# Performance work log

Hardware: AMD Instinct MI355X
Metric: run time of the kernel (lower is better)

The kernel has to match this reference:

```python
import jax, jax.numpy as jnp
import numpy as np

HIDDEN = 4096
N_HEADS = 32
N_KV = 8
HEAD_DIM = 128
ROPE_BASE = 10000.0


def setup_inputs() -> dict:
    key = jax.random.key(0)
    k0, k1, k2, k3, k4 = jax.random.split(key, 5)
    B, S = 1, 2048
    scale = 0.02
    return {
        "hidden_states": jax.random.normal(k0, (B, S, HIDDEN), dtype=jnp.float32),
        "Wq": jax.random.normal(k1, (N_HEADS * HEAD_DIM, HIDDEN), dtype=jnp.float32) * scale,
        "Wk": jax.random.normal(k2, (N_KV * HEAD_DIM, HIDDEN), dtype=jnp.float32) * scale,
        "Wv": jax.random.normal(k3, (N_KV * HEAD_DIM, HIDDEN), dtype=jnp.float32) * scale,
        "Wo": jax.random.normal(k4, (HIDDEN, N_HEADS * HEAD_DIM), dtype=jnp.float32) * scale,
    }


def _rotate_half(x):
    x1, x2 = jnp.split(x, 2, axis=-1)
    return jnp.concatenate([-x2, x1], axis=-1)


def _rope_cos_sin(seq_len, dtype):
    inv_freq = 1.0 / (ROPE_BASE ** (jnp.arange(0, HEAD_DIM, 2, dtype=jnp.float32) / HEAD_DIM))
    t = jnp.arange(seq_len, dtype=jnp.float32)
    freqs = jnp.outer(t, inv_freq)                 # [S, hd/2]
    emb = jnp.concatenate([freqs, freqs], axis=-1) # [S, hd]
    return jnp.cos(emb).astype(dtype), jnp.sin(emb).astype(dtype)


def reference(hidden_states, Wq, Wk, Wv, Wo):
    B, S, _ = hidden_states.shape
    scale = HEAD_DIM ** -0.5
    groups = N_HEADS // N_KV

    q = (hidden_states @ Wq.T).reshape(B, S, N_HEADS, HEAD_DIM).transpose(0, 2, 1, 3)
    k = (hidden_states @ Wk.T).reshape(B, S, N_KV, HEAD_DIM).transpose(0, 2, 1, 3)
    v = (hidden_states @ Wv.T).reshape(B, S, N_KV, HEAD_DIM).transpose(0, 2, 1, 3)

    cos, sin = _rope_cos_sin(S, q.dtype)           # [S, hd] each, broadcast over (B, H)
    q = q * cos + _rotate_half(q) * sin
    k = k * cos + _rotate_half(k) * sin

    # repeat_kv: [B, nkv, S, hd] -> [B, nkv*groups, S, hd]
    k = jnp.broadcast_to(k[:, :, None], (B, N_KV, groups, S, HEAD_DIM)).reshape(B, N_HEADS, S, HEAD_DIM)
    v = jnp.broadcast_to(v[:, :, None], (B, N_KV, groups, S, HEAD_DIM)).reshape(B, N_HEADS, S, HEAD_DIM)

    scores = jnp.einsum('bhqd,bhkd->bhqk', q, k) * scale
    causal = jnp.tril(jnp.ones((S, S), dtype=bool))
    scores = jnp.where(causal, scores, -jnp.inf)
    probs = jax.nn.softmax(scores.astype(jnp.float32), axis=-1).astype(q.dtype)

    attn = jnp.einsum('bhqk,bhkd->bhqd', probs, v)            # [B, H, S, hd]
    attn = attn.transpose(0, 2, 1, 3).reshape(B, S, N_HEADS * HEAD_DIM)
    return attn @ Wo.T
```

## Files before the change

kernel.cpp:

```cpp
#include <hip/hip_runtime.h>
#include <hip/hip_bf16.h>
#include <math.h>

#define S_LEN 2048
#define HIDDEN 4096
#define N_HEADS 32
#define N_KV 8
#define HEAD_DIM 128

typedef __attribute__((ext_vector_type(8))) short short8;
typedef __attribute__((ext_vector_type(4))) float f32x4;

typedef __attribute__((address_space(3))) unsigned int as3_u32;
typedef const __attribute__((address_space(1))) unsigned int as1_u32;

__device__ __forceinline__ void gload16(const void* g, void* lds) {
  __builtin_amdgcn_global_load_lds((as1_u32*)g, (as3_u32*)lds, 16, 0, 0);
}

__device__ __forceinline__ unsigned short f2bf(float f) {
  unsigned int u = __float_as_uint(f);
  return (unsigned short)((u + 0x7fff + ((u >> 16) & 1)) >> 16);
}
__device__ __forceinline__ float bf2f(unsigned short u) {
  return __uint_as_float(((unsigned int)u) << 16);
}

__global__ void conv_bf16(const float* __restrict__ in, unsigned short* __restrict__ out, int n) {
  int i = (blockIdx.x * blockDim.x + threadIdx.x) * 4;
  if (i >= n) return;
  float4 v = *(const float4*)&in[i];
  ushort4 o;
  o.x = f2bf(v.x); o.y = f2bf(v.y); o.z = f2bf(v.z); o.w = f2bf(v.w);
  *(ushort4*)&out[i] = o;
}

__device__ __forceinline__ void storeC(float* C, float v) { *C = v; }
__device__ __forceinline__ void storeC(unsigned short* C, float v) { *C = f2bf(v); }

template <typename OutT>
__device__ __forceinline__ void gemm_core_128(
    const unsigned short* __restrict__ A, const unsigned short* __restrict__ B,
    OutT* __restrict__ C, int K, int ldc) {
  __shared__ unsigned short As[128 * 32];
  __shared__ unsigned short Bs[128 * 32];

  const int tid = threadIdx.x;
  const int w = tid >> 6;
  const int lane = tid & 63;
  const int wr = (w >> 1) * 64;
  const int wc = (w & 1) * 64;
  const int lrow = lane & 15;
  const int lk8 = lane >> 4;

  f32x4 acc[4][4];
#pragma unroll
  for (int i = 0; i < 4; i++)
#pragma unroll
    for (int j = 0; j < 4; j++) acc[i][j] = (f32x4){0.f, 0.f, 0.f, 0.f};

  const int sr = (lane >> 2);
  const int sc = (lane & 3) * 8;

  for (int k0 = 0; k0 < K; k0 += 32) {
    __syncthreads();
#pragma unroll
    for (int s = 0; s < 2; s++) {
      int r = w * 32 + s * 16 + sr;
      gload16(&A[(size_t)r * K + k0 + sc], &As[(w * 32 + s * 16) * 32]);
      gload16(&B[(size_t)r * K + k0 + sc], &Bs[(w * 32 + s * 16) * 32]);
    }
    __syncthreads();

    short8 a[4], b[4];
#pragma unroll
    for (int i = 0; i < 4; i++)
      a[i] = *(const short8*)&As[(wr + i * 16 + lrow) * 32 + lk8 * 8];
#pragma unroll
    for (int j = 0; j < 4; j++)
      b[j] = *(const short8*)&Bs[(wc + j * 16 + lrow) * 32 + lk8 * 8];
#pragma unroll
    for (int i = 0; i < 4; i++)
#pragma unroll
      for (int j = 0; j < 4; j++)
        acc[i][j] = __builtin_amdgcn_mfma_f32_16x16x32_bf16(a[i], b[j], acc[i][j], 0, 0, 0);
  }

#pragma unroll
  for (int i = 0; i < 4; i++)
#pragma unroll
    for (int j = 0; j < 4; j++) {
      int col = wc + j * 16 + lrow;
#pragma unroll
      for (int r = 0; r < 4; r++) {
        int row = wr + i * 16 + lk8 * 4 + r;
        storeC(&C[(size_t)row * ldc + col], acc[i][j][r]);
      }
    }
}

__global__ __launch_bounds__(256) void gemm_qkv(
    const unsigned short* __restrict__ Xb,
    const unsigned short* __restrict__ Wqb, const unsigned short* __restrict__ Wkb,
    const unsigned short* __restrict__ Wvb,
    unsigned short* __restrict__ Qb, unsigned short* __restrict__ Kb,
    unsigned short* __restrict__ Vb) {
  const int colBase = blockIdx.x * 128;
  const int rowBase = blockIdx.y * 128;
  const unsigned short* B;
  unsigned short* C;
  int ldc, ccol;
  if (colBase < 4096)      { B = Wqb + (size_t)colBase * HIDDEN;          C = Qb; ldc = 4096; ccol = colBase; }
  else if (colBase < 5120) { B = Wkb + (size_t)(colBase - 4096) * HIDDEN; C = Kb; ldc = 1024; ccol = colBase - 4096; }
  else                     { B = Wvb + (size_t)(colBase - 5120) * HIDDEN; C = Vb; ldc = 1024; ccol = colBase - 5120; }
  gemm_core_128(Xb + (size_t)rowBase * HIDDEN, B,
                C + (size_t)rowBase * ldc + ccol, HIDDEN, ldc);
}

__global__ __launch_bounds__(256) void gemm_out(
    const unsigned short* __restrict__ Ob, const unsigned short* __restrict__ Wob,
    float* __restrict__ C) {
  const int colBase = blockIdx.x * 128;
  const int rowBase = blockIdx.y * 128;
  gemm_core_128(Ob + (size_t)rowBase * HIDDEN, Wob + (size_t)colBase * HIDDEN,
                C + (size_t)rowBase * HIDDEN + colBase, HIDDEN, HIDDEN);
}

#define QSCALE 0.12753102123752056f

__global__ void rope_kernel(const unsigned short* __restrict__ Q,
                            const unsigned short* __restrict__ K,
                            unsigned short* __restrict__ Qp,
                            unsigned short* __restrict__ Kp) {
  int idx = blockIdx.x * blockDim.x + threadIdx.x;
  int d = idx & 63;
  int sh = idx >> 6;
  int h = sh % (N_HEADS + N_KV);
  int s = sh / (N_HEADS + N_KV);
  if (s >= S_LEN) return;

  float freq = expf(-(float)d * (9.210340371976184f / 64.0f));
  float ang = (float)s * freq;
  float sn, cs;
  sincosf(ang, &sn, &cs);

  const unsigned short* src;
  unsigned short* dst;
  float sc_out;
  if (h < N_HEADS) {
    src = Q + ((size_t)s * N_HEADS + h) * HEAD_DIM;
    dst = Qp + (((size_t)h * 128 + (s >> 4)) * 16 + (s & 15)) * HEAD_DIM;
    sc_out = QSCALE;
  } else {
    int kvh = h - N_HEADS;
    src = K + ((size_t)s * N_KV + kvh) * HEAD_DIM;
    dst = Kp + (((size_t)kvh * 32 + (s >> 6)) * 64 + (s & 63)) * HEAD_DIM;
    sc_out = 1.0f;
  }

  float x1 = bf2f(src[d]);
  float x2 = bf2f(src[d + 64]);
  dst[d] = f2bf((x1 * cs - x2 * sn) * sc_out);
  dst[d + 64] = f2bf((x2 * cs + x1 * sn) * sc_out);
}

__global__ __launch_bounds__(256) void transp_v(
    const unsigned short* __restrict__ Vb, unsigned short* __restrict__ Vp) {
  __shared__ unsigned short t[64][72];
  const int s0 = blockIdx.x * 64;
  const int c0 = blockIdx.y * 64;
  const int kt = s0 >> 6;
  const int tid = threadIdx.x;
#pragma unroll
  for (int i = 0; i < 2; i++) {
    int c = tid + i * 256;
    int r = c >> 3, ch = c & 7;
    *(short8*)&t[r][ch * 8] = *(const short8*)&Vb[(size_t)(s0 + r) * 1024 + c0 + ch * 8];
  }
  __syncthreads();
#pragma unroll
  for (int i = 0; i < 4; i++) {
    int c = tid + i * 256;
    int orow = c >> 4, oc4 = (c & 15) * 4;
    int g = c0 + orow;
    int kvh = g >> 7, d = g & 127;
    ushort4 o;
    o.x = t[oc4 + 0][orow]; o.y = t[oc4 + 1][orow];
    o.z = t[oc4 + 2][orow]; o.w = t[oc4 + 3][orow];
    *(ushort4*)&Vp[(((size_t)kvh * 32 + kt) * 128 + d) * 64 + oc4] = o;
  }
}

#define AK 64

__global__ __launch_bounds__(256, 4) void attn_mfma(
    const unsigned short* __restrict__ Qp, const unsigned short* __restrict__ Kp,
    const unsigned short* __restrict__ Vp, unsigned short* __restrict__ Ob) {
  const int b = blockIdx.x;
  const int h = b & 31;
  const int j = b >> 5;
  const int qt = (b < 512) ? j : (47 - j);
  const int kvh = h >> 2;

  const int tid = threadIdx.x;
  const int w = tid >> 6;
  const int lane = tid & 63;
  const int lrow = lane & 15;
  const int lk8 = lane >> 4;

  __shared__ unsigned short Ks[64 * 128];
  __shared__ unsigned short Vts[128 * 64];
  __shared__ unsigned short Ps[4 * 16 * 64];
  unsigned short* Pw = &Ps[w * 16 * 64];

  short8 qf[4];
  const int t0 = qt * 4 + w;
#pragma unroll
  for (int ks = 0; ks < 4; ks++)
    qf[ks] = *(const short8*)&Qp[(((size_t)h * 128 + t0) * 16 + lrow) * 128 +
                                 ks * 32 + lk8 * 8];

  f32x4 acc[8];
  float m_i = -1e30f, l_i = 0.f;
#pragma unroll
  for (int n = 0; n < 8; n++) acc[n] = (f32x4){0.f, 0.f, 0.f, 0.f};

  const int nkt = qt + 1;

  for (int kt = 0; kt < nkt; kt++) {
    const int kb = kt * AK;
    const unsigned short* Kt  = Kp + ((size_t)kvh * 32 + kt) * 8192;
    const unsigned short* Vtt = Vp + ((size_t)kvh * 32 + kt) * 8192;

    __syncthreads();
#pragma unroll
    for (int jj = 0; jj < 4; jj++) {
      int seg = w * 4 + jj;
      int kr = seg * 4 + lk8;
      int kc = lrow ^ (kr & 15);
      gload16(Kt + ((size_t)kr * 16 + kc) * 8, &Ks[seg * 512]);
      int vr = seg * 8 + (lane >> 3);
      int vc = (lane & 7) ^ (vr & 7);
      gload16(Vtt + ((size_t)vr * 8 + vc) * 8, &Vts[seg * 512]);
    }
    __syncthreads();

    f32x4 s[4];
#pragma unroll
    for (int n = 0; n < 4; n++) s[n] = (f32x4){0.f, 0.f, 0.f, 0.f};

#pragma unroll
    for (int ks = 0; ks < 4; ks++) {
      short8 kf[4];
#pragma unroll
      for (int n = 0; n < 4; n++)
        kf[n] = *(const short8*)&Ks[(n * 16 + lrow) * 128 + (((ks * 4 + lk8) ^ lrow)) * 8];
#pragma unroll
      for (int n = 0; n < 4; n++)
        s[n] = __builtin_amdgcn_mfma_f32_16x16x32_bf16(kf[n], qf[ks], s[n], 0, 0, 0);
    }

    const int wqb = qt * 64 + w * 16;
    if (kb + AK - 1 > wqb) {
      int query = wqb + lrow;
#pragma unroll
      for (int n = 0; n < 4; n++) {
        int keyb = kb + n * 16 + lk8 * 4;
#pragma unroll
        for (int r = 0; r < 4; r++)
          if (keyb + r > query) s[n][r] = -1e30f;
      }
    }

    {
      float mx = -1e30f;
#pragma unroll
      for (int n = 0; n < 4; n++)
#pragma unroll
        for (int r = 0; r < 4; r++) mx = fmaxf(mx, s[n][r]);
      mx = fmaxf(mx, __shfl_xor(mx, 16, 64));
      mx = fmaxf(mx, __shfl_xor(mx, 32, 64));
      float mn = fmaxf(m_i, mx);
      float al = exp2f(m_i - mn);
      m_i = mn;
      float ls = 0.f;
#pragma unroll
      for (int n = 0; n < 4; n++)
#pragma unroll
        for (int r = 0; r < 4; r++) {
          float e = exp2f(s[n][r] - mn);
          s[n][r] = e;
          ls += e;
        }
      ls += __shfl_xor(ls, 16, 64);
      ls += __shfl_xor(ls, 32, 64);
      l_i = l_i * al + ls;
#pragma unroll
      for (int n = 0; n < 8; n++)
#pragma unroll
        for (int r = 0; r < 4; r++) acc[n][r] *= al;
    }

#pragma unroll
    for (int n = 0; n < 4; n++) {
      ushort4 pk;
      pk.x = f2bf(s[n][0]); pk.y = f2bf(s[n][1]);
      pk.z = f2bf(s[n][2]); pk.w = f2bf(s[n][3]);
      int c8 = n * 4 + lk8;
      int c16s = (c8 >> 1) ^ (lrow & 7);
      *(ushort4*)&Pw[lrow * 64 + c16s * 8 + (c8 & 1) * 4] = pk;
    }

#pragma unroll
    for (int ks2 = 0; ks2 < 2; ks2++) {
      int c16s = (ks2 * 4 + lk8) ^ (lrow & 7);
      short8 pf = *(const short8*)&Pw[lrow * 64 + c16s * 8];
#pragma unroll
      for (int n = 0; n < 8; n++) {
        short8 vf = *(const short8*)&Vts[(n * 16 + lrow) * 64 +
                                         (((ks2 * 4 + lk8) ^ (lrow & 7))) * 8];
        acc[n] = __builtin_amdgcn_mfma_f32_16x16x32_bf16(vf, pf, acc[n], 0, 0, 0);
      }
    }
  }

  {
    float inv = 1.0f / l_i;
    int row = qt * 64 + w * 16 + lrow;
#pragma unroll
    for (int n = 0; n < 8; n++) {
      ushort4 o;
      o.x = f2bf(acc[n][0] * inv); o.y = f2bf(acc[n][1] * inv);
      o.z = f2bf(acc[n][2] * inv); o.w = f2bf(acc[n][3] * inv);
      *(ushort4*)&Ob[(size_t)row * 4096 + h * 128 + n * 16 + lk8 * 4] = o;
    }
  }
}

extern "C" void kernel_launch(void* const* d_in, const int* in_sizes, int n_in,
                              void* d_out, int out_size, void* d_ws, size_t ws_size,
                              hipStream_t stream) {
  const float* X  = (const float*)d_in[0];
  const float* Wq = (const float*)d_in[1];
  const float* Wk = (const float*)d_in[2];
  const float* Wv = (const float*)d_in[3];
  const float* Wo = (const float*)d_in[4];
  float* out = (float*)d_out;

  char* p = (char*)d_ws;
  unsigned short* Qb  = (unsigned short*)p; p += (size_t)S_LEN * 4096 * 2;
  unsigned short* Kb  = (unsigned short*)p; p += (size_t)S_LEN * 1024 * 2;
  unsigned short* Vb  = (unsigned short*)p; p += (size_t)S_LEN * 1024 * 2;
  unsigned short* Qp  = (unsigned short*)p; p += (size_t)S_LEN * 4096 * 2;
  unsigned short* Kp  = (unsigned short*)p; p += (size_t)S_LEN * 1024 * 2;
  unsigned short* Vp  = (unsigned short*)p; p += (size_t)S_LEN * 1024 * 2;
  unsigned short* Xb  = (unsigned short*)p; p += (size_t)S_LEN * 4096 * 2;
  unsigned short* Wqb = (unsigned short*)p; p += (size_t)4096 * 4096 * 2;
  unsigned short* Wkb = (unsigned short*)p; p += (size_t)1024 * 4096 * 2;
  unsigned short* Wvb = (unsigned short*)p; p += (size_t)1024 * 4096 * 2;
  unsigned short* Ob  = Xb;
  unsigned short* Wob = Wqb;

  conv_bf16<<<(S_LEN * 4096 / 4 + 255) / 256, 256, 0, stream>>>(X, Xb, S_LEN * 4096);
  conv_bf16<<<(4096 * 4096 / 4 + 255) / 256, 256, 0, stream>>>(Wq, Wqb, 4096 * 4096);
  conv_bf16<<<(1024 * 4096 / 4 + 255) / 256, 256, 0, stream>>>(Wk, Wkb, 1024 * 4096);
  conv_bf16<<<(1024 * 4096 / 4 + 255) / 256, 256, 0, stream>>>(Wv, Wvb, 1024 * 4096);

  gemm_qkv<<<dim3(6144 / 128, S_LEN / 128), 256, 0, stream>>>(Xb, Wqb, Wkb, Wvb, Qb, Kb, Vb);

  int rope_threads = S_LEN * (N_HEADS + N_KV) * 64;
  rope_kernel<<<rope_threads / 256, 256, 0, stream>>>(Qb, Kb, Qp, Kp);

  transp_v<<<dim3(S_LEN / 64, 1024 / 64), 256, 0, stream>>>(Vb, Vp);

  conv_bf16<<<(4096 * 4096 / 4 + 255) / 256, 256, 0, stream>>>(Wo, Wob, 4096 * 4096);

  attn_mfma<<<1024, 256, 0, stream>>>(Qp, Kp, Vp, Ob);

  gemm_out<<<dim3(4096 / 128, S_LEN / 128), 256, 0, stream>>>(Ob, Wob, out);
}
```

Baseline: 507.5 us.

## Rewrite GEMM core as 256x128 triple-buffered pipeline with swizzled LDS

Replaces the 128x128, BK=32 single-buffered GEMM core with a 256x128 tile using BK=64, 512 threads and a three-stage LDS ring. Tiles k+2 are loaded asynchronously with global_load_lds while MFMAs run on the current stage. LDS columns are XOR-swizzled to avoid bank conflicts, and MFMA sections are raised in priority with s_setprio. The goal is to hide global memory latency and raise MFMA utilisation in the QKV and output projections. The cost is about 147KB of LDS per block, which limits occupancy to one block per CU despite the launch bound.

```diff
diff --git a/kernel.cpp b/kernel.cpp
--- a/kernel.cpp
+++ b/kernel.cpp
@@ -38,20 +38,28 @@
 __device__ __forceinline__ void storeC(float* C, float v) { *C = v; }
 __device__ __forceinline__ void storeC(unsigned short* C, float v) { *C = f2bf(v); }
 
+#define BM 256
+#define BN 128
+#define BK 64
+#define NKT (HIDDEN / BK)
+
 template <typename OutT>
-__device__ __forceinline__ void gemm_core_128(
-    const unsigned short* __restrict__ A, const unsigned short* __restrict__ B,
-    OutT* __restrict__ C, int K, int ldc) {
-  __shared__ unsigned short As[128 * 32];
-  __shared__ unsigned short Bs[128 * 32];
+__device__ __forceinline__ void gemm_core_256x128(
+    const unsigned short* __restrict__ A,
+    const unsigned short* __restrict__ B,
+    OutT* __restrict__ C, int ldc) {
+  __shared__ unsigned short Abuf[3][BM * BK];
+  __shared__ unsigned short Bbuf[3][BN * BK];
 
   const int tid = threadIdx.x;
   const int w = tid >> 6;
   const int lane = tid & 63;
+  const int lrow = lane & 15;
+  const int lk8 = lane >> 4;
   const int wr = (w >> 1) * 64;
   const int wc = (w & 1) * 64;
-  const int lrow = lane & 15;
-  const int lk8 = lane >> 4;
+  const int lr8 = lane >> 3;
+  const int lp = lane & 7;
 
   f32x4 acc[4][4];
 #pragma unroll
@@ -59,32 +67,87 @@
 #pragma unroll
     for (int j = 0; j < 4; j++) acc[i][j] = (f32x4){0.f, 0.f, 0.f, 0.f};
 
-  const int sr = (lane >> 2);
-  const int sc = (lane & 3) * 8;
-
-  for (int k0 = 0; k0 < K; k0 += 32) {
-    __syncthreads();
-#pragma unroll
-    for (int s = 0; s < 2; s++) {
-      int r = w * 32 + s * 16 + sr;
-      gload16(&A[(size_t)r * K + k0 + sc], &As[(w * 32 + s * 16) * 32]);
-      gload16(&B[(size_t)r * K + k0 + sc], &Bs[(w * 32 + s * 16) * 32]);
-    }
-    __syncthreads();
-
-    short8 a[4], b[4];
-#pragma unroll
-    for (int i = 0; i < 4; i++)
-      a[i] = *(const short8*)&As[(wr + i * 16 + lrow) * 32 + lk8 * 8];
-#pragma unroll
-    for (int j = 0; j < 4; j++)
-      b[j] = *(const short8*)&Bs[(wc + j * 16 + lrow) * 32 + lk8 * 8];
-#pragma unroll
-    for (int i = 0; i < 4; i++)
-#pragma unroll
-      for (int j = 0; j < 4; j++)
-        acc[i][j] = __builtin_amdgcn_mfma_f32_16x16x32_bf16(a[i], b[j], acc[i][j], 0, 0, 0);
-  }
+#define STAGE_A(bi, t, g) {                                                  \
+    int seg = (g) * 8 + w;                                                   \
+    int r = seg * 8 + lr8;                                                   \
+    int c = lp ^ (r & 7);                                                    \
+    gload16(&A[(size_t)r * HIDDEN + (t) * BK + c * 8], &Abuf[bi][seg * 512]);\
+  }
+#define STAGE_B(bi, t, g) {                                                  \
+    int seg = (g) * 8 + w;                                                   \
+    int r = seg * 8 + lr8;                                                   \
+    int c = lp ^ (r & 7);                                                    \
+    gload16(&B[(size_t)r * HIDDEN + (t) * BK + c * 8], &Bbuf[bi][seg * 512]);\
+  }
+#define RD_FRAG(buf, rbase, ks)                                              \
+  (*(const short8*)&(buf)[((rbase) + lrow) * 64 + (((ks) * 4 + lk8) ^ (((rbase) + lrow) & 7)) * 8])
+
+#pragma unroll
+  for (int g = 0; g < 4; g++) STAGE_A(0, 0, g);
+#pragma unroll
+  for (int g = 0; g < 2; g++) STAGE_B(0, 0, g);
+#pragma unroll
+  for (int g = 0; g < 4; g++) STAGE_A(1, 1, g);
+#pragma unroll
+  for (int g = 0; g < 2; g++) STAGE_B(1, 1, g);
+  asm volatile("s_waitcnt vmcnt(6)" ::: "memory");
+  __builtin_amdgcn_s_barrier();
+
+  for (int t = 0; t < NKT; t++) {
+    const int bi = t % 3;
+    const int bs = (t + 2) % 3;
+    const bool st = (t + 2) < NKT;
+    const unsigned short* Ac = Abuf[bi];
+    const unsigned short* Bc = Bbuf[bi];
+
+    short8 bfr[4][2], afr[2][2];
+
+#pragma unroll
+    for (int n = 0; n < 4; n++)
+#pragma unroll
+      for (int ks = 0; ks < 2; ks++)
+        bfr[n][ks] = RD_FRAG(Bc, wc + n * 16, ks);
+#pragma unroll
+    for (int m = 0; m < 2; m++)
+#pragma unroll
+      for (int ks = 0; ks < 2; ks++)
+        afr[m][ks] = RD_FRAG(Ac, wr + m * 16, ks);
+    if (st) { STAGE_A(bs, t + 2, 0); STAGE_A(bs, t + 2, 1); STAGE_B(bs, t + 2, 0); }
+    __builtin_amdgcn_s_barrier();
+    __builtin_amdgcn_s_setprio(1);
+#pragma unroll
+    for (int m = 0; m < 2; m++)
+#pragma unroll
+      for (int n = 0; n < 4; n++)
+#pragma unroll
+        for (int ks = 0; ks < 2; ks++)
+          acc[m][n] = __builtin_amdgcn_mfma_f32_16x16x32_bf16(afr[m][ks], bfr[n][ks], acc[m][n], 0, 0, 0);
+    __builtin_amdgcn_s_setprio(0);
+    __builtin_amdgcn_s_barrier();
+
+#pragma unroll
+    for (int m = 0; m < 2; m++)
+#pragma unroll
+      for (int ks = 0; ks < 2; ks++)
+        afr[m][ks] = RD_FRAG(Ac, wr + (m + 2) * 16, ks);
+    if (st) { STAGE_A(bs, t + 2, 2); STAGE_A(bs, t + 2, 3); STAGE_B(bs, t + 2, 1); }
+    __builtin_amdgcn_s_barrier();
+    __builtin_amdgcn_s_setprio(1);
+#pragma unroll
+    for (int m = 0; m < 2; m++)
+#pragma unroll
+      for (int n = 0; n < 4; n++)
+#pragma unroll
+        for (int ks = 0; ks < 2; ks++)
+          acc[m + 2][n] = __builtin_amdgcn_mfma_f32_16x16x32_bf16(afr[m][ks], bfr[n][ks], acc[m + 2][n], 0, 0, 0);
+    __builtin_amdgcn_s_setprio(0);
+    if (st) asm volatile("s_waitcnt vmcnt(6)" ::: "memory");
+    else    asm volatile("s_waitcnt vmcnt(0)" ::: "memory");
+    __builtin_amdgcn_s_barrier();
+  }
+#undef STAGE_A
+#undef STAGE_B
+#undef RD_FRAG
 
 #pragma unroll
   for (int i = 0; i < 4; i++)
@@ -99,31 +162,31 @@
     }
 }
 
-__global__ __launch_bounds__(256) void gemm_qkv(
+__global__ __launch_bounds__(512, 2) void gemm_qkv(
     const unsigned short* __restrict__ Xb,
     const unsigned short* __restrict__ Wqb, const unsigned short* __restrict__ Wkb,
     const unsigned short* __restrict__ Wvb,
     unsigned short* __restrict__ Qb, unsigned short* __restrict__ Kb,
     unsigned short* __restrict__ Vb) {
-  const int colBase = blockIdx.x * 128;
-  const int rowBase = blockIdx.y * 128;
+  const int colBase = blockIdx.x * BN;
+  const int rowBase = blockIdx.y * BM;
   const unsigned short* B;
   unsigned short* C;
   int ldc, ccol;
   if (colBase < 4096)      { B = Wqb + (size_t)colBase * HIDDEN;          C = Qb; ldc = 4096; ccol = colBase; }
   else if (colBase < 5120) { B = Wkb + (size_t)(colBase - 4096) * HIDDEN; C = Kb; ldc = 1024; ccol = colBase - 4096; }
   else                     { B = Wvb + (size_t)(colBase - 5120) * HIDDEN; C = Vb; ldc = 1024; ccol = colBase - 5120; }
-  gemm_core_128(Xb + (size_t)rowBase * HIDDEN, B,
-                C + (size_t)rowBase * ldc + ccol, HIDDEN, ldc);
-}
-
-__global__ __launch_bounds__(256) void gemm_out(
+  gemm_core_256x128(Xb + (size_t)rowBase * HIDDEN, B,
+                    C + (size_t)rowBase * ldc + ccol, ldc);
+}
+
+__global__ __launch_bounds__(512, 2) void gemm_out(
     const unsigned short* __restrict__ Ob, const unsigned short* __restrict__ Wob,
     float* __restrict__ C) {
-  const int colBase = blockIdx.x * 128;
-  const int rowBase = blockIdx.y * 128;
-  gemm_core_128(Ob + (size_t)rowBase * HIDDEN, Wob + (size_t)colBase * HIDDEN,
-                C + (size_t)rowBase * HIDDEN + colBase, HIDDEN, HIDDEN);
+  const int colBase = blockIdx.x * BN;
+  const int rowBase = blockIdx.y * BM;
+  gemm_core_256x128(Ob + (size_t)rowBase * HIDDEN, Wob + (size_t)colBase * HIDDEN,
+                    C + (size_t)rowBase * HIDDEN + colBase, HIDDEN);
 }
 
 #define QSCALE 0.12753102123752056f
@@ -366,7 +429,7 @@
   conv_bf16<<<(1024 * 4096 / 4 + 255) / 256, 256, 0, stream>>>(Wk, Wkb, 1024 * 4096);
   conv_bf16<<<(1024 * 4096 / 4 + 255) / 256, 256, 0, stream>>>(Wv, Wvb, 1024 * 4096);
 
-  gemm_qkv<<<dim3(6144 / 128, S_LEN / 128), 256, 0, stream>>>(Xb, Wqb, Wkb, Wvb, Qb, Kb, Vb);
+  gemm_qkv<<<dim3(6144 / BN, S_LEN / BM), 512, 0, stream>>>(Xb, Wqb, Wkb, Wvb, Qb, Kb, Vb);
 
   int rope_threads = S_LEN * (N_HEADS + N_KV) * 64;
   rope_kernel<<<rope_threads / 256, 256, 0, stream>>>(Qb, Kb, Qp, Kp);
@@ -377,5 +440,5 @@
 
   attn_mfma<<<1024, 256, 0, stream>>>(Qp, Kp, Vp, Ob);
 
-  gemm_out<<<dim3(4096 / 128, S_LEN / 128), 256, 0, stream>>>(Ob, Wob, out);
-}
+  gemm_out<<<dim3(4096 / BN, S_LEN / BM), 512, 0, stream>>>(Ob, Wob, out);
+}
```

Measured after the change: 493.4 us. 1.03x faster.
